# Kernel tuning notes

Measured on AMD Instinct MI355X. Metric: run time of the kernel, lower is better.

The kernel has to match this reference:

```python
import jax, jax.numpy as jnp
import numpy as np

WIN = 64
SHIFT = 32
HEADS = 12


def setup_inputs() -> dict:
    key = jax.random.key(0)
    ks = jax.random.split(key, 6)
    D = 768
    return {
        'x': jax.random.normal(ks[0], (16, 4096, D), dtype=jnp.float32),
        'qkv_w': jax.random.normal(ks[1], (3 * D, D), dtype=jnp.float32) * (D ** -0.5),
        'qkv_b': jax.random.normal(ks[2], (3 * D,), dtype=jnp.float32) * 0.02,
        'proj_w': jax.random.normal(ks[3], (D, D), dtype=jnp.float32) * (D ** -0.5),
        'proj_b': jax.random.normal(ks[4], (D,), dtype=jnp.float32) * 0.02,
        'rel_bias': jax.random.normal(ks[5], (HEADS, 2 * WIN - 1), dtype=jnp.float32) * 0.02,
    }


def reference(x, qkv_w, qkv_b, proj_w, proj_b, rel_bias):
    B, N, D = x.shape
    H, hd = HEADS, D // HEADS
    scale = hd ** -0.5
    if SHIFT:
        x = jnp.roll(x, SHIFT, axis=1)
    pad = (-N) % WIN
    if pad:
        x = jnp.pad(x, ((0, 0), (0, pad), (0, 0)))
    Np = x.shape[1]
    nW = Np // WIN
    # [B*nW, w, D] windows
    xw = x.reshape(B * nW, WIN, D)
    qkv = xw @ qkv_w.T + qkv_b                       # [B*nW, w, 3D]
    qkv = qkv.reshape(B * nW, WIN, 3, H, hd).transpose(2, 0, 3, 1, 4)
    q, k, v = qkv[0], qkv[1], qkv[2]                 # [B*nW, H, w, hd]
    attn = jnp.einsum('bhqd,bhkd->bhqk', q, k) * scale
    idx = jnp.arange(WIN)
    rel = idx[None, :] - idx[:, None] + (WIN - 1)    # [w, w] in [0, 2w-2]
    attn = attn + rel_bias[:, rel][None]             # gather bias per head
    attn = jax.nn.softmax(attn, axis=-1)
    y = jnp.einsum('bhqk,bhkd->bhqd', attn, v)       # [B*nW, H, w, hd]
    y = y.transpose(0, 2, 1, 3).reshape(B * nW, WIN, D)
    y = y @ proj_w.T + proj_b
    y = y.reshape(B, Np, D)
    if pad:
        y = y[:, :N, :]
    if SHIFT:
        y = jnp.roll(y, -SHIFT, axis=1)
    return y
```

## Files before the change

### kernel.cpp

```cpp
#include <hip/hip_runtime.h>
#include <hip/hip_bf16.h>
#include <stdint.h>

#define SEQ     4096
#define NBATCH  16
#define DMODEL  768
#define NHEAD   12
#define HDIM    64
#define WINSZ   64
#define SHIFT_T 32
#define QKV_N   (3*DMODEL)

typedef __attribute__((ext_vector_type(8)))  short bf16x8;
typedef __attribute__((ext_vector_type(4)))  float f32x4;

static __device__ __forceinline__ unsigned short f2bf(float f) {
  union { float f; unsigned u; } v; v.f = f;
  unsigned r = v.u + 0x7fffu + ((v.u >> 16) & 1u);
  return (unsigned short)(r >> 16);
}

#define G2L(gp, lp) __builtin_amdgcn_global_load_lds( \
    (const __attribute__((address_space(1))) unsigned*)(const void*)(gp), \
    (__attribute__((address_space(3))) unsigned*)(void*)(lp), 16, 0, 0)

#define MFMA16(a,b,c) __builtin_amdgcn_mfma_f32_16x16x32_bf16(a,b,c,0,0,0)
#define LDS8(p) (*(const bf16x8*)(p))
#define BARR __builtin_amdgcn_s_barrier()
#define SBAR __builtin_amdgcn_sched_barrier(0)
#define LGK0 do { asm volatile("s_waitcnt lgkmcnt(0)" ::: "memory"); SBAR; } while(0)

__global__ void k_cvt_x(const float* __restrict__ x, unsigned short* __restrict__ xb,
                        long long c0, long long n8) {
  for (long long i = (long long)blockIdx.x*blockDim.x + threadIdx.x; i < n8;
       i += (long long)gridDim.x*blockDim.x) {
    long long e = i*8;
    int d = (int)(e % DMODEL);
    long long gt = c0 + e / DMODEL;
    int t = (int)(gt & (SEQ-1));
    long long b = gt >> 12;
    int ts = (t - SHIFT_T) & (SEQ-1);
    const float* src = x + (((b << 12) + ts) * (long long)DMODEL + d);
    float4 a0 = *(const float4*)src;
    float4 a1 = *(const float4*)(src + 4);
    bf16x8 o;
    o[0]=(short)f2bf(a0.x); o[1]=(short)f2bf(a0.y); o[2]=(short)f2bf(a0.z); o[3]=(short)f2bf(a0.w);
    o[4]=(short)f2bf(a1.x); o[5]=(short)f2bf(a1.y); o[6]=(short)f2bf(a1.z); o[7]=(short)f2bf(a1.w);
    *(bf16x8*)(xb + e) = o;
  }
}

__global__ void k_cvt_w(const float* __restrict__ w, unsigned short* __restrict__ wb, int n8) {
  int i = blockIdx.x*blockDim.x + threadIdx.x;
  if (i >= n8) return;
  float4 a0 = ((const float4*)w)[2*i];
  float4 a1 = ((const float4*)w)[2*i+1];
  bf16x8 o;
  o[0]=(short)f2bf(a0.x); o[1]=(short)f2bf(a0.y); o[2]=(short)f2bf(a0.z); o[3]=(short)f2bf(a0.w);
  o[4]=(short)f2bf(a1.x); o[5]=(short)f2bf(a1.y); o[6]=(short)f2bf(a1.z); o[7]=(short)f2bf(a1.w);
  ((bf16x8*)wb)[i] = o;
}

template<int MODE>
__global__ __launch_bounds__(512, 1)
void k_gemm256(const unsigned short* __restrict__ A, const unsigned short* __restrict__ Bw,
               const float* __restrict__ bias, unsigned short* __restrict__ Cb,
               float* __restrict__ Cf, int M, int N, int K, int nTN, long long c0) {
  __shared__ char lds[131072];
  const int nt = K >> 6;
  int nwg = gridDim.x;
  int cpx = nwg >> 3;
  int wg  = (blockIdx.x & 7) * cpx + (blockIdx.x >> 3);
  int bm = wg / nTN, bn = wg - bm*nTN;
  long long m0 = (long long)bm * 256;
  int n0 = bn * 256;
  int tid = threadIdx.x;
  int lane = tid & 63, wid = tid >> 6;
  int wr = wid >> 2, wc = wid & 3;
  int cl = lane & 15, g4 = lane >> 4;

  const long long K2 = 2LL * K;
  int L  = tid * 16;
  int Ls = L ^ (((L >> 7) & 7) << 4);
  int srow = Ls >> 7, scol = Ls & 127;
  const char* gAr0 = (const char*)A + (m0 +       srow) * K2 + scol;
  const char* gAr1 = (const char*)A + (m0 +  64 + srow) * K2 + scol;
  const char* gAr2 = (const char*)A + (m0 + 128 + srow) * K2 + scol;
  const char* gAr3 = (const char*)A + (m0 + 192 + srow) * K2 + scol;
  const char* gBr0 = (const char*)Bw + (long long)(n0 +       srow) * K2 + scol;
  const char* gBr1 = (const char*)Bw + (long long)(n0 +  64 + srow) * K2 + scol;
  const char* gBr2 = (const char*)Bw + (long long)(n0 + 128 + srow) * K2 + scol;
  const char* gBr3 = (const char*)Bw + (long long)(n0 + 192 + srow) * K2 + scol;

  int p0 = cl*128 + ((g4*16) ^ ((cl & 7) << 4));
  int p1 = p0 ^ 64;
  int RA0 = wr*16384;
  int RA1 = wr*16384 + 8192;
  int BB  = 32768 + wc*8192;

  f32x4 acc[8][4];
  #pragma unroll
  for (int i = 0; i < 8; ++i)
    #pragma unroll
    for (int j = 0; j < 4; ++j) acc[i][j] = (f32x4){0.f,0.f,0.f,0.f};

#define MMPH(MA, MB, x0, x1, y0, y1) \
  acc[MA][0]=MFMA16(x0,b00,acc[MA][0]); acc[MA][1]=MFMA16(x0,b10,acc[MA][1]); \
  acc[MA][2]=MFMA16(x0,b20,acc[MA][2]); acc[MA][3]=MFMA16(x0,b30,acc[MA][3]); \
  acc[MB][0]=MFMA16(y0,b00,acc[MB][0]); acc[MB][1]=MFMA16(y0,b10,acc[MB][1]); \
  acc[MB][2]=MFMA16(y0,b20,acc[MB][2]); acc[MB][3]=MFMA16(y0,b30,acc[MB][3]); \
  acc[MA][0]=MFMA16(x1,b01,acc[MA][0]); acc[MA][1]=MFMA16(x1,b11,acc[MA][1]); \
  acc[MA][2]=MFMA16(x1,b21,acc[MA][2]); acc[MA][3]=MFMA16(x1,b31,acc[MA][3]); \
  acc[MB][0]=MFMA16(y1,b01,acc[MB][0]); acc[MB][1]=MFMA16(y1,b11,acc[MB][1]); \
  acc[MB][2]=MFMA16(y1,b21,acc[MB][2]); acc[MB][3]=MFMA16(y1,b31,acc[MB][3]);

#define TILE(RD, ST, DOSTAGE, WBSTR, DOWA) do {                               \
    const char* rbuf = (RD); char* stb = (ST);                                \
    bf16x8 b00,b01,b10,b11,b20,b21,b30,b31;                                   \
    { bf16x8 x0 = LDS8(rbuf + RA0        + p0), x1 = LDS8(rbuf + RA0        + p1);\
      bf16x8 y0 = LDS8(rbuf + RA0 + 2048 + p0), y1 = LDS8(rbuf + RA0 + 2048 + p1);\
      b00 = LDS8(rbuf + BB        + p0);  b01 = LDS8(rbuf + BB        + p1);  \
      b10 = LDS8(rbuf + BB + 2048 + p0);  b11 = LDS8(rbuf + BB + 2048 + p1);  \
      b20 = LDS8(rbuf + BB + 4096 + p0);  b21 = LDS8(rbuf + BB + 4096 + p1);  \
      b30 = LDS8(rbuf + BB + 6144 + p0);  b31 = LDS8(rbuf + BB + 6144 + p1);  \
      if (DOSTAGE) { G2L(gBr0, stb + 32768 + L); G2L(gBr1, stb + 40960 + L); }\
      asm volatile("s_waitcnt lgkmcnt(8)" ::: "memory"); SBAR;                \
      BARR; LGK0;                                                             \
      __builtin_amdgcn_s_setprio(1);                                          \
      MMPH(0, 1, x0, x1, y0, y1)                                              \
      __builtin_amdgcn_s_setprio(0); SBAR; BARR;                              \
    }                                                                         \
    { bf16x8 x0 = LDS8(rbuf + RA0 + 4096 + p0), x1 = LDS8(rbuf + RA0 + 4096 + p1);\
      bf16x8 y0 = LDS8(rbuf + RA0 + 6144 + p0), y1 = LDS8(rbuf + RA0 + 6144 + p1);\
      if (DOSTAGE) { G2L(gBr2, stb + 49152 + L); G2L(gBr3, stb + 57344 + L); }\
      SBAR; BARR; LGK0;                                                       \
      __builtin_amdgcn_s_setprio(1);                                          \
      MMPH(2, 3, x0, x1, y0, y1)                                              \
      __builtin_amdgcn_s_setprio(0); SBAR;                                    \
      asm volatile(WBSTR ::: "memory"); SBAR; BARR;                           \
    }                                                                         \
    { bf16x8 x0 = LDS8(rbuf + RA1        + p0), x1 = LDS8(rbuf + RA1        + p1);\
      bf16x8 y0 = LDS8(rbuf + RA1 + 2048 + p0), y1 = LDS8(rbuf + RA1 + 2048 + p1);\
      if (DOSTAGE) { G2L(gAr0, stb + L); G2L(gAr2, stb + 16384 + L); }        \
      SBAR; BARR; LGK0;                                                       \
      __builtin_amdgcn_s_setprio(1);                                          \
      MMPH(4, 5, x0, x1, y0, y1)                                              \
      __builtin_amdgcn_s_setprio(0); SBAR; BARR;                              \
    }                                                                         \
    { bf16x8 x0 = LDS8(rbuf + RA1 + 4096 + p0), x1 = LDS8(rbuf + RA1 + 4096 + p1);\
      bf16x8 y0 = LDS8(rbuf + RA1 + 6144 + p0), y1 = LDS8(rbuf + RA1 + 6144 + p1);\
      if (DOSTAGE) { G2L(gAr1, stb + 8192 + L); G2L(gAr3, stb + 24576 + L);   \
                     gAr0 += 128; gAr1 += 128; gAr2 += 128; gAr3 += 128;      \
                     gBr0 += 128; gBr1 += 128; gBr2 += 128; gBr3 += 128; }    \
      SBAR; BARR; LGK0;                                                       \
      __builtin_amdgcn_s_setprio(1);                                          \
      MMPH(6, 7, x0, x1, y0, y1)                                              \
      __builtin_amdgcn_s_setprio(0); SBAR;                                    \
      if (DOWA) { asm volatile("s_waitcnt vmcnt(2)" ::: "memory"); }          \
      SBAR; BARR;                                                             \
    }                                                                         \
  } while (0)

  G2L(gBr0, lds + 32768 + L); G2L(gBr1, lds + 40960 + L);
  G2L(gBr2, lds + 49152 + L); G2L(gBr3, lds + 57344 + L);
  G2L(gAr0, lds + L);         G2L(gAr2, lds + 16384 + L);
  G2L(gAr1, lds + 8192 + L);  G2L(gAr3, lds + 24576 + L);
  gAr0 += 128; gAr1 += 128; gAr2 += 128; gAr3 += 128;
  gBr0 += 128; gBr1 += 128; gBr2 += 128; gBr3 += 128;
  asm volatile("s_waitcnt vmcnt(2)" ::: "memory");
  SBAR; BARR;

  char* const bufA = lds;
  char* const bufB = lds + 65536;
  for (int i = 0; i < (nt - 2) / 2; ++i) {
    TILE(bufA, bufB, 1, "s_waitcnt vmcnt(4)", 1);
    TILE(bufB, bufA, 1, "s_waitcnt vmcnt(4)", 1);
  }
  TILE(bufA, bufB, 1, "s_waitcnt vmcnt(4)", 1);
  TILE(bufB, bufA, 0, "s_waitcnt vmcnt(0)", 0);
#undef TILE
#undef MMPH

  #pragma unroll
  for (int mf = 0; mf < 8; ++mf) {
    #pragma unroll
    for (int nf = 0; nf < 4; ++nf) {
      int n = n0 + wc*64 + nf*16 + cl;
      float bv = bias[n];
      #pragma unroll
      for (int r = 0; r < 4; ++r) {
        long long m = m0 + wr*128 + mf*16 + g4*4 + r;
        float v = acc[mf][nf][r] + bv;
        if (MODE == 0) {
          Cb[m * (long long)N + n] = f2bf(v);
        } else {
          long long gm = c0 + m;
          long long om = (gm & ~(long long)(SEQ-1)) | ((gm - SHIFT_T) & (long long)(SEQ-1));
          Cf[om * (long long)N + n] = v;
        }
      }
    }
  }
}

__global__ __launch_bounds__(256, 4)
void k_attn(const unsigned short* __restrict__ qkv, const float* __restrict__ rel_bias,
            unsigned short* __restrict__ y) {
  int w = blockIdx.x / NHEAD;
  int h = blockIdx.x - w*NHEAD;
  __shared__ unsigned short sQ[64*72], sK[64*72], sV[64*72];
  __shared__ unsigned short sP[4][16*72];
  __shared__ float rb[128];
  int tid = threadIdx.x, lane = tid & 63, wid = tid >> 6;
  int cl = lane & 15, g4 = lane >> 4;

  if (tid < 2*WINSZ - 1) rb[tid] = rel_bias[h*(2*WINSZ-1) + tid];

  const unsigned short* base = qkv + (long long)w*WINSZ*QKV_N + h*HDIM;
  #pragma unroll
  for (int pass = 0; pass < 2; ++pass) {
    int row = (tid >> 3) + pass*32;
    int ch  = tid & 7;
    const unsigned short* src = base + (long long)row*QKV_N + ch*8;
    *(bf16x8*)(sQ + row*72 + ch*8) = *(const bf16x8*)(src);
    *(bf16x8*)(sK + row*72 + ch*8) = *(const bf16x8*)(src + DMODEL);
    *(bf16x8*)(sV + row*72 + ch*8) = *(const bf16x8*)(src + 2*DMODEL);
  }
  __syncthreads();

  f32x4 sc[4];
  #pragma unroll
  for (int nt = 0; nt < 4; ++nt) sc[nt] = (f32x4){0.f,0.f,0.f,0.f};
  #pragma unroll
  for (int kk = 0; kk < 2; ++kk) {
    bf16x8 aq = *(const bf16x8*)(sQ + (wid*16 + cl)*72 + kk*32 + g4*8);
    #pragma unroll
    for (int nt = 0; nt < 4; ++nt) {
      bf16x8 bk = *(const bf16x8*)(sK + (nt*16 + cl)*72 + kk*32 + g4*8);
      sc[nt] = MFMA16(aq, bk, sc[nt]);
    }
  }

  float pv[4][4];
  #pragma unroll
  for (int r = 0; r < 4; ++r) {
    int qi = wid*16 + g4*4 + r;
    float mx = -1e30f;
    #pragma unroll
    for (int nt = 0; nt < 4; ++nt) {
      int kj = nt*16 + cl;
      float v = sc[nt][r]*0.125f + rb[kj - qi + (WINSZ-1)];
      pv[nt][r] = v;
      mx = fmaxf(mx, v);
    }
    #pragma unroll
    for (int m = 1; m < 16; m <<= 1) mx = fmaxf(mx, __shfl_xor(mx, m, 64));
    float sum = 0.f;
    #pragma unroll
    for (int nt = 0; nt < 4; ++nt) { float e = __expf(pv[nt][r]-mx); pv[nt][r] = e; sum += e; }
    #pragma unroll
    for (int m = 1; m < 16; m <<= 1) sum += __shfl_xor(sum, m, 64);
    float inv = 1.f / sum;
    #pragma unroll
    for (int nt = 0; nt < 4; ++nt)
      sP[wid][(g4*4+r)*72 + nt*16 + cl] = f2bf(pv[nt][r]*inv);
  }

  f32x4 o[4];
  #pragma unroll
  for (int nt = 0; nt < 4; ++nt) o[nt] = (f32x4){0.f,0.f,0.f,0.f};
  #pragma unroll
  for (int kk = 0; kk < 2; ++kk) {
    bf16x8 ap = *(const bf16x8*)(&sP[wid][cl*72 + kk*32 + g4*8]);
    #pragma unroll
    for (int nt = 0; nt < 4; ++nt) {
      bf16x8 bv;
      #pragma unroll
      for (int j = 0; j < 8; ++j)
        bv[j] = (short)sV[(kk*32 + g4*8 + j)*72 + nt*16 + cl];
      o[nt] = MFMA16(ap, bv, o[nt]);
    }
  }

  long long tokbase = (long long)w * WINSZ;
  #pragma unroll
  for (int nt = 0; nt < 4; ++nt)
    #pragma unroll
    for (int r = 0; r < 4; ++r) {
      int row = wid*16 + g4*4 + r;
      y[(tokbase + row) * (long long)DMODEL + h*HDIM + nt*16 + cl] = f2bf(o[nt][r]);
    }
}

extern "C" void kernel_launch(void* const* d_in, const int* in_sizes, int n_in,
                              void* d_out, int out_size, void* d_ws, size_t ws_size,
                              hipStream_t stream) {
  const float* x      = (const float*)d_in[0];
  const float* qkv_w  = (const float*)d_in[1];
  const float* qkv_b  = (const float*)d_in[2];
  const float* proj_w = (const float*)d_in[3];
  const float* proj_b = (const float*)d_in[4];
  const float* rel_b  = (const float*)d_in[5];
  float* out = (float*)d_out;

  const long long NTOK = (long long)NBATCH * SEQ;
  const size_t wbytes = (size_t)QKV_N*DMODEL*2 + (size_t)DMODEL*DMODEL*2;
  const size_t ybytes = (size_t)NTOK*DMODEL*2;

  int C = 16;
  for (int c : {2, 4, 8, 16}) {
    size_t tpc = (size_t)NTOK / c;
    size_t need = tpc*QKV_N*2 + ybytes + wbytes;
    if (need <= ws_size) { C = c; break; }
  }
  long long tpc = NTOK / C;

  char* ws = (char*)d_ws;
  unsigned short* qkvb = (unsigned short*)ws;
  unsigned short* yb   = (unsigned short*)(ws + (size_t)tpc*QKV_N*2);
  unsigned short* wq   = (unsigned short*)(ws + (size_t)tpc*QKV_N*2 + ybytes);
  unsigned short* wp   = wq + (size_t)QKV_N*DMODEL;

  k_cvt_w<<<(QKV_N*DMODEL/8 + 255)/256, 256, 0, stream>>>(qkv_w, wq, QKV_N*DMODEL/8);
  k_cvt_w<<<(DMODEL*DMODEL/8 + 255)/256, 256, 0, stream>>>(proj_w, wp, DMODEL*DMODEL/8);

  for (int c = 0; c < C; ++c) {
    long long c0 = (long long)c * tpc;
    unsigned short* xb = yb + (size_t)c0 * DMODEL;
    long long n8 = tpc * DMODEL / 8;
    int cvtGrid = (int)((n8 + 255) / 256); if (cvtGrid > 2048) cvtGrid = 2048;
    k_cvt_x<<<cvtGrid, 256, 0, stream>>>(x, xb, c0, n8);

    int mT = (int)(tpc / 256);
    k_gemm256<0><<<mT * (QKV_N/256), 512, 0, stream>>>(xb, wq, qkv_b, qkvb, nullptr,
                                                       (int)tpc, QKV_N, DMODEL, QKV_N/256, c0);
    k_attn<<<(int)(tpc/WINSZ) * NHEAD, 256, 0, stream>>>(qkvb, rel_b, xb );
  }
  int mT = (int)(NTOK / 256);
  k_gemm256<1><<<mT * (DMODEL/256), 512, 0, stream>>>(yb, wp, proj_b, nullptr, out,
                                                      (int)NTOK, DMODEL, DMODEL, DMODEL/256, 0);
}
```

Before: 505.4 us.

## Store QKV in per-window-head panels and drop chunked launches

The QKV GEMM epilogue now writes its output as contiguous 64x64 panels per (window, head, q/k/v), so the attention kernel loads each tile with fully contiguous reads instead of strided rows. The chunking loop that sized work to the workspace is removed, and each stage is now a single launch over all tokens, which cuts launch count. This assumes the workspace holds the full QKV buffer; if it is too small the code will overrun it. The epilogue's panel stores are 16-element runs, which may coalesce less well than full-row writes.

```diff
diff --git a/kernel.cpp b/kernel.cpp
--- a/kernel.cpp
+++ b/kernel.cpp
@@ -31,12 +31,12 @@
 #define LGK0 do { asm volatile("s_waitcnt lgkmcnt(0)" ::: "memory"); SBAR; } while(0)
 
 __global__ void k_cvt_x(const float* __restrict__ x, unsigned short* __restrict__ xb,
-                        long long c0, long long n8) {
+                        long long n8) {
   for (long long i = (long long)blockIdx.x*blockDim.x + threadIdx.x; i < n8;
        i += (long long)gridDim.x*blockDim.x) {
     long long e = i*8;
     int d = (int)(e % DMODEL);
-    long long gt = c0 + e / DMODEL;
+    long long gt = e / DMODEL;
     int t = (int)(gt & (SEQ-1));
     long long b = gt >> 12;
     int ts = (t - SHIFT_T) & (SEQ-1);
@@ -192,7 +192,11 @@
         long long m = m0 + wr*128 + mf*16 + g4*4 + r;
         float v = acc[mf][nf][r] + bv;
         if (MODE == 0) {
-          Cb[m * (long long)N + n] = f2bf(v);
+          int nb = n0 + wc*64;
+          int t  = nb / DMODEL;
+          int h  = (nb - t*DMODEL) >> 6;
+          long long panel = ((((m >> 6)*NHEAD + h)*3 + t) << 12);
+          Cb[panel + ((m & 63) << 6) + nf*16 + cl] = f2bf(v);
         } else {
           long long gm = c0 + m;
           long long om = (gm & ~(long long)(SEQ-1)) | ((gm - SHIFT_T) & (long long)(SEQ-1));
@@ -216,15 +220,16 @@
 
   if (tid < 2*WINSZ - 1) rb[tid] = rel_bias[h*(2*WINSZ-1) + tid];
 
-  const unsigned short* base = qkv + (long long)w*WINSZ*QKV_N + h*HDIM;
-  #pragma unroll
-  for (int pass = 0; pass < 2; ++pass) {
-    int row = (tid >> 3) + pass*32;
-    int ch  = tid & 7;
-    const unsigned short* src = base + (long long)row*QKV_N + ch*8;
-    *(bf16x8*)(sQ + row*72 + ch*8) = *(const bf16x8*)(src);
-    *(bf16x8*)(sK + row*72 + ch*8) = *(const bf16x8*)(src + DMODEL);
-    *(bf16x8*)(sV + row*72 + ch*8) = *(const bf16x8*)(src + 2*DMODEL);
+  const unsigned short* panel = qkv + ((long long)((w*NHEAD + h)*3) << 12);
+  {
+    int row = tid >> 2, c16 = (tid & 3) * 16;
+    const unsigned short* s0 = panel + tid*16;
+    *(bf16x8*)(sQ + row*72 + c16)     = *(const bf16x8*)(s0);
+    *(bf16x8*)(sQ + row*72 + c16 + 8) = *(const bf16x8*)(s0 + 8);
+    *(bf16x8*)(sK + row*72 + c16)     = *(const bf16x8*)(s0 + 4096);
+    *(bf16x8*)(sK + row*72 + c16 + 8) = *(const bf16x8*)(s0 + 4096 + 8);
+    *(bf16x8*)(sV + row*72 + c16)     = *(const bf16x8*)(s0 + 8192);
+    *(bf16x8*)(sV + row*72 + c16 + 8) = *(const bf16x8*)(s0 + 8192 + 8);
   }
   __syncthreads();
 
@@ -304,39 +309,23 @@
   float* out = (float*)d_out;
 
   const long long NTOK = (long long)NBATCH * SEQ;
-  const size_t wbytes = (size_t)QKV_N*DMODEL*2 + (size_t)DMODEL*DMODEL*2;
-  const size_t ybytes = (size_t)NTOK*DMODEL*2;
-
-  int C = 16;
-  for (int c : {2, 4, 8, 16}) {
-    size_t tpc = (size_t)NTOK / c;
-    size_t need = tpc*QKV_N*2 + ybytes + wbytes;
-    if (need <= ws_size) { C = c; break; }
-  }
-  long long tpc = NTOK / C;
 
   char* ws = (char*)d_ws;
   unsigned short* qkvb = (unsigned short*)ws;
-  unsigned short* yb   = (unsigned short*)(ws + (size_t)tpc*QKV_N*2);
-  unsigned short* wq   = (unsigned short*)(ws + (size_t)tpc*QKV_N*2 + ybytes);
+  unsigned short* yb   = (unsigned short*)(ws + (size_t)NTOK*QKV_N*2);
+  unsigned short* wq   = (unsigned short*)(ws + (size_t)NTOK*QKV_N*2 + (size_t)NTOK*DMODEL*2);
   unsigned short* wp   = wq + (size_t)QKV_N*DMODEL;
 
   k_cvt_w<<<(QKV_N*DMODEL/8 + 255)/256, 256, 0, stream>>>(qkv_w, wq, QKV_N*DMODEL/8);
   k_cvt_w<<<(DMODEL*DMODEL/8 + 255)/256, 256, 0, stream>>>(proj_w, wp, DMODEL*DMODEL/8);
 
-  for (int c = 0; c < C; ++c) {
-    long long c0 = (long long)c * tpc;
-    unsigned short* xb = yb + (size_t)c0 * DMODEL;
-    long long n8 = tpc * DMODEL / 8;
-    int cvtGrid = (int)((n8 + 255) / 256); if (cvtGrid > 2048) cvtGrid = 2048;
-    k_cvt_x<<<cvtGrid, 256, 0, stream>>>(x, xb, c0, n8);
-
-    int mT = (int)(tpc / 256);
-    k_gemm256<0><<<mT * (QKV_N/256), 512, 0, stream>>>(xb, wq, qkv_b, qkvb, nullptr,
-                                                       (int)tpc, QKV_N, DMODEL, QKV_N/256, c0);
-    k_attn<<<(int)(tpc/WINSZ) * NHEAD, 256, 0, stream>>>(qkvb, rel_b, xb );
-  }
+  long long n8 = NTOK * DMODEL / 8;
+  k_cvt_x<<<2048, 256, 0, stream>>>(x, yb , n8);
+
   int mT = (int)(NTOK / 256);
+  k_gemm256<0><<<mT * (QKV_N/256), 512, 0, stream>>>(yb, wq, qkv_b, qkvb, nullptr,
+                                                     (int)NTOK, QKV_N, DMODEL, QKV_N/256, 0);
+  k_attn<<<(int)(NTOK/WINSZ) * NHEAD, 256, 0, stream>>>(qkvb, rel_b, yb );
   k_gemm256<1><<<mT * (DMODEL/256), 512, 0, stream>>>(yb, wp, proj_b, nullptr, out,
                                                       (int)NTOK, DMODEL, DMODEL, DMODEL/256, 0);
 }
```

New measurement: 498.6 us, median of 2. Within noise of the previous version (-1.3%).
